# Optimization experiments

Measured on AMD Instinct MI355X. Metric: run time of the kernel, lower is better.

Reference implementation:

```python
import jax, jax.numpy as jnp
import numpy as np
from jax.scipy.special import logsumexp

EPS = 0.05        # entropic regularization (blur^p)
N_ITERS = 20      # Sinkhorn iterations
N, M, D = 8192, 8192, 64


def setup_inputs() -> dict:
    key = jax.random.key(0)
    k1, k2, k3, k4 = jax.random.split(key, 4)
    return {
        "a": jax.random.uniform(k1, (N,), dtype=jnp.float32),
        "x": jax.random.normal(k2, (N, D), dtype=jnp.float32),
        "b": jax.random.uniform(k3, (M,), dtype=jnp.float32),
        "y": jax.random.normal(k4, (M, D), dtype=jnp.float32),
    }


def reference(a, x, b, y):
    eps = EPS
    # _normalize_weights: probability simplex
    a = a / jnp.sum(a)
    b = b / jnp.sum(b)
    loga = jnp.log(a)
    logb = jnp.log(b)
    # squared-Euclidean cost C_ij = ||x_i - y_j||^2, built via one GEMM (online kernel's math)
    x2 = jnp.sum(x * x, axis=1)            # [N]
    y2 = jnp.sum(y * y, axis=1)            # [M]
    C = x2[:, None] + y2[None, :] - 2.0 * (x @ y.T)   # [N, M]

    # log-domain Sinkhorn: f_i = -eps * LSE_j( log b_j + (g_j - C_ij)/eps )
    def softmin_rows(g_, C_, logw):   # reduce over columns j -> [N]
        return -eps * logsumexp(logw[None, :] + (g_[None, :] - C_) / eps, axis=1)

    def softmin_cols(f_, C_, logw):   # reduce over rows i -> [M]
        return -eps * logsumexp(logw[:, None] + (f_[:, None] - C_) / eps, axis=0)

    def body(i, fg):
        f_, g_ = fg
        f_ = softmin_rows(g_, C, logb)
        g_ = softmin_cols(f_, C, loga)
        return (f_, g_)

    f0 = jnp.zeros_like(a)
    g0 = jnp.zeros_like(b)
    f, g = jax.lax.fori_loop(0, N_ITERS, body, (f0, g0))

    # GeomLoss-style: one final symmetric update from detached potentials (Danskin)
    f_d = jax.lax.stop_gradient(f)
    g_d = jax.lax.stop_gradient(g)
    f_fin = softmin_rows(g_d, C, logb)
    g_fin = softmin_cols(f_d, C, loga)
    # OT_eps(a, b) = <a, f> + <b, g>
    return jnp.sum(a * f_fin) + jnp.sum(b * g_fin)
```

## Files before the change

kernel.cpp:

```cpp
#include <hip/hip_runtime.h>
#include <hip/hip_bf16.h>

#define EPS       0.05f
#define N_ITERS   20
#define NR        8192
#define DIM       64
#define LOG2E     1.4426950408889634f
#define LN2       0.6931471805599453f
#define S2        (2.0f * LOG2E / EPS)
#define EPSLN2    (EPS * LN2)
#define NEGINF    (-1e30f)
#define NSPLIT    16

typedef __attribute__((ext_vector_type(8))) short short8;
typedef __attribute__((ext_vector_type(4))) float float4v;

#define GLD_LDS16(src, dst)                                              \
    __builtin_amdgcn_global_load_lds(                                    \
        (const __attribute__((address_space(1))) void*)(src),            \
        (__attribute__((address_space(3))) void*)(dst), 16, 0, 0)

__device__ __forceinline__ float wave_reduce_sum(float v) {
    #pragma unroll
    for (int m = 1; m < 64; m <<= 1) v += __shfl_xor(v, m, 64);
    return v;
}

__device__ __forceinline__ float merge16_l(const float2* __restrict__ P, int i) {
    float2 p[NSPLIT];
    float M = NEGINF;
    #pragma unroll
    for (int k = 0; k < NSPLIT; k++) {
        p[k] = P[k * NR + i];
        M = fmaxf(M, p[k].x);
    }
    float S = 0.f;
    #pragma unroll
    for (int k = 0; k < NSPLIT; k++)
        S += p[k].y * __builtin_amdgcn_exp2f(p[k].x - M);
    return M + __builtin_amdgcn_logf(S);
}

__global__ void sums_kernel(const float* __restrict__ a, const float* __restrict__ b,
                            float* __restrict__ sums) {
    __shared__ float red[32];
    int tid = threadIdx.x;
    float pa = 0.f, pb = 0.f;
    for (int i = tid; i < NR; i += blockDim.x) { pa += a[i]; pb += b[i]; }
    pa = wave_reduce_sum(pa);
    pb = wave_reduce_sum(pb);
    int wid = tid >> 6, ln = tid & 63;
    if (ln == 0) { red[wid] = pa; red[wid + 16] = pb; }
    __syncthreads();
    if (tid == 0) {
        float sa = 0.f, sb = 0.f;
        int nw = blockDim.x >> 6;
        for (int w = 0; w < nw; w++) { sa += red[w]; sb += red[w + 16]; }
        sums[0] = logf(sa); sums[1] = logf(sb); sums[2] = sa; sums[3] = sb;
    }
}

__global__ void prep_kernel(const float* __restrict__ x, const float* __restrict__ y,
                            const float* __restrict__ a, const float* __restrict__ b,
                            const float* __restrict__ sums,
                            short8* __restrict__ xs, short8* __restrict__ ys,
                            float* __restrict__ x2, float* __restrict__ y2,
                            float* __restrict__ la2, float* __restrict__ lb2,
                            float2* __restrict__ Pb) {
    int gid = blockIdx.x * 256 + threadIdx.x;
    bool isx = gid < NR * 8;
    int cid = isx ? gid : gid - NR * 8;
    int row = cid >> 3;
    int c   = cid & 7;
    const float4* src = (const float4*)(isx ? x : y);
    float4 v0 = src[row * 16 + c * 2];
    float4 v1 = src[row * 16 + c * 2 + 1];

    short8 st;
    st[0] = __bfloat16_as_short(__float2bfloat16(v0.x));
    st[1] = __bfloat16_as_short(__float2bfloat16(v0.y));
    st[2] = __bfloat16_as_short(__float2bfloat16(v0.z));
    st[3] = __bfloat16_as_short(__float2bfloat16(v0.w));
    st[4] = __bfloat16_as_short(__float2bfloat16(v1.x));
    st[5] = __bfloat16_as_short(__float2bfloat16(v1.y));
    st[6] = __bfloat16_as_short(__float2bfloat16(v1.z));
    st[7] = __bfloat16_as_short(__float2bfloat16(v1.w));

    int T = row >> 4, ln = row & 15, f = c >> 2, q = c & 3;
    (isx ? xs : ys)[T * 128 + f * 64 + q * 16 + ln] = st;

    float sq = v0.x*v0.x + v0.y*v0.y + v0.z*v0.z + v0.w*v0.w
             + v1.x*v1.x + v1.y*v1.y + v1.z*v1.z + v1.w*v1.w;
    #pragma unroll
    for (int m = 1; m < 8; m <<= 1) sq += __shfl_xor(sq, m, 64);

    if (c == 0) {
        if (isx) {
            x2[row] = sq;
            la2[row] = (logf(a[row]) - sums[0]) * LOG2E;
        } else {
            y2[row] = sq;
            lb2[row] = (logf(b[row]) - sums[1]) * LOG2E;
            Pb[row] = make_float2(sq * (LOG2E / EPS), 1.0f);
            #pragma unroll
            for (int k = 1; k < NSPLIT; k++)
                Pb[k * NR + row] = make_float2(NEGINF, 0.0f);
        }
    }
}

#define LSE4(acc, c4, mm, ss)                                            \
    {                                                                    \
        float z0 = fmaf(S2, (acc)[0], (c4).x);                           \
        float z1 = fmaf(S2, (acc)[1], (c4).y);                           \
        float z2 = fmaf(S2, (acc)[2], (c4).z);                           \
        float z3 = fmaf(S2, (acc)[3], (c4).w);                           \
        float zm = fmaxf(fmaxf(z0, z1), fmaxf(z2, z3));                  \
        float mn = fmaxf((mm), zm);                                      \
        float e  = __builtin_amdgcn_exp2f((mm) - mn);                    \
        float p  = (__builtin_amdgcn_exp2f(z0 - mn)                      \
                  + __builtin_amdgcn_exp2f(z1 - mn))                     \
                 + (__builtin_amdgcn_exp2f(z2 - mn)                      \
                  + __builtin_amdgcn_exp2f(z3 - mn));                    \
        (ss) = fmaf((ss), e, p);                                         \
        (mm) = mn;                                                       \
    }

__global__ __launch_bounds__(1024, 4) void pass_kernel(
        const short8* __restrict__ matXs,
        const short8* __restrict__ matYs,
        const float2* __restrict__ Pin,
        const float* __restrict__ lw2col,
        float2* __restrict__ Pout) {
    __shared__ __attribute__((aligned(16))) char xlds[65536];
    __shared__ __attribute__((aligned(16))) char ybuf[2][16384];
    __shared__ __attribute__((aligned(16))) float cbl[512];
    __shared__ float2 comb[512][5];

    const int tid = threadIdx.x;
    const int bi  = blockIdx.x;
    const int q   = bi & 15;
    const int rg  = bi >> 4;
    const int rb  = rg * 512;
    const int cb0 = q * 512;

    const int w    = tid >> 6;
    const int lane = tid & 63;
    const int quad = lane >> 4;
    const int ln   = lane & 15;
    const int cst  = w & 3;
    const int rq   = w >> 2;

    const char* xsrc = (const char*)matXs + (size_t)rb * 128;
    #pragma unroll
    for (int r = 0; r < 4; r++)
        GLD_LDS16(xsrc + r * 16384 + tid * 16, &xlds[r * 16384 + w * 1024]);
    const char* ysrc = (const char*)matYs + (size_t)cb0 * 128;
    GLD_LDS16(ysrc + 0 * 16384 + tid * 16, &ybuf[0][w * 1024]);
    GLD_LDS16(ysrc + 1 * 16384 + tid * 16, &ybuf[1][w * 1024]);
    __builtin_amdgcn_sched_barrier(0);

    if (tid < 512) {
        int j = cb0 + tid;
        cbl[tid] = lw2col[j] - merge16_l(Pin, j);
    }
    __builtin_amdgcn_sched_barrier(0);
    __builtin_amdgcn_s_waitcnt(0x0071);
    __builtin_amdgcn_s_barrier();
    __builtin_amdgcn_sched_barrier(0);

    short8 xf0[8], xf1[8];
    {
        const char* xw = &xlds[(rq * 8) * 2048];
        #pragma unroll
        for (int t = 0; t < 8; t++) {
            xf0[t] = *(const short8*)(xw + t * 2048 + lane * 16);
            xf1[t] = *(const short8*)(xw + t * 2048 + 1024 + lane * 16);
        }
    }

    float lm[8], ls[8];
    #pragma unroll
    for (int t = 0; t < 8; t++) { lm[t] = NEGINF; ls[t] = 0.f; }

    #pragma unroll
    for (int c = 0; c < 4; c++) {
        const char* base = &ybuf[c & 1][0];
        #pragma unroll
        for (int uu = 0; uu < 2; uu++) {
            const int u = cst * 2 + uu;
            short8 ya0 = *(const short8*)(base + u * 2048 + lane * 16);
            short8 ya1 = *(const short8*)(base + u * 2048 + 1024 + lane * 16);
            float4 c4  = *(const float4*)(cbl + (c * 8 + u) * 16 + quad * 4);

            #pragma unroll
            for (int tt = 0; tt < 8; tt++) {
                float4v acc = {0.f, 0.f, 0.f, 0.f};
                acc = __builtin_amdgcn_mfma_f32_16x16x32_bf16(ya0, xf0[tt], acc, 0, 0, 0);
                acc = __builtin_amdgcn_mfma_f32_16x16x32_bf16(ya1, xf1[tt], acc, 0, 0, 0);
                LSE4(acc, c4, lm[tt], ls[tt]);
            }
        }
        if (c < 3) {
            __builtin_amdgcn_sched_barrier(0);
            __builtin_amdgcn_s_barrier();
            __builtin_amdgcn_sched_barrier(0);
            if (c < 2)
                GLD_LDS16(ysrc + (c + 2) * 16384 + tid * 16, &ybuf[c & 1][w * 1024]);
            __builtin_amdgcn_sched_barrier(0);
            if (c < 2) __builtin_amdgcn_s_waitcnt(0x0071);
            else       __builtin_amdgcn_s_waitcnt(0x0070);
            __builtin_amdgcn_s_barrier();
            __builtin_amdgcn_sched_barrier(0);
        }
    }

    #pragma unroll
    for (int mask = 16; mask < 64; mask <<= 1) {
        #pragma unroll
        for (int t = 0; t < 8; t++) {
            float mo = __shfl_xor(lm[t], mask, 64);
            float so = __shfl_xor(ls[t], mask, 64);
            float M  = fmaxf(lm[t], mo);
            ls[t] = ls[t] * __builtin_amdgcn_exp2f(lm[t] - M)
                  + so    * __builtin_amdgcn_exp2f(mo    - M);
            lm[t] = M;
        }
    }

    __syncthreads();
    if (lane < 16) {
        #pragma unroll
        for (int t = 0; t < 8; t++)
            comb[rq * 128 + t * 16 + ln][cst] = make_float2(lm[t], ls[t]);
    }
    __syncthreads();

    if (tid < 512) {
        float2 cc0 = comb[tid][0];
        float M = cc0.x, S = cc0.y;
        #pragma unroll
        for (int cc = 1; cc < 4; cc++) {
            float2 p = comb[tid][cc];
            float Mn = fmaxf(M, p.x);
            S = S * __builtin_amdgcn_exp2f(M - Mn)
              + p.y * __builtin_amdgcn_exp2f(p.x - Mn);
            M = Mn;
        }
        Pout[q * NR + rb + tid] = make_float2(M, S);
    }
}

__global__ void reduce1_kernel(const float* __restrict__ a, const float* __restrict__ b,
                               const float* __restrict__ x2, const float* __restrict__ y2,
                               const float2* __restrict__ Pff, const float2* __restrict__ Pgf,
                               float2* __restrict__ red2) {
    __shared__ float red[4];
    int tid = threadIdx.x;
    int r   = blockIdx.x * 128 + (tid & 127);
    bool gs = tid >= 128;
    float L  = merge16_l(gs ? Pgf : Pff, r);
    float sq = gs ? y2[r] : x2[r];
    float wv = gs ? b[r]  : a[r];
    float v  = wv * (sq - EPSLN2 * L);
    v = wave_reduce_sum(v);
    if ((tid & 63) == 0) red[tid >> 6] = v;
    __syncthreads();
    if (tid == 0) red2[blockIdx.x] = make_float2(red[0] + red[1], red[2] + red[3]);
}

__global__ void reduce2_kernel(const float* __restrict__ sums,
                               const float2* __restrict__ red2,
                               float* __restrict__ out) {
    int tid = threadIdx.x;
    float2 v = red2[tid];
    float da = wave_reduce_sum(v.x);
    float db = wave_reduce_sum(v.y);
    if (tid == 0) out[0] = da / sums[2] + db / sums[3];
}

extern "C" void kernel_launch(void* const* d_in, const int* in_sizes, int n_in,
                              void* d_out, int out_size, void* d_ws, size_t ws_size,
                              hipStream_t stream) {
    const float* a = (const float*)d_in[0];
    const float* x = (const float*)d_in[1];
    const float* b = (const float*)d_in[2];
    const float* y = (const float*)d_in[3];

    char* ws = (char*)d_ws;
    short8* xs = (short8*)ws;
    short8* ys = (short8*)(ws + (1 << 20));
    float* fp  = (float*)(ws + (2 << 20));
    float* x2  = fp;
    float* y2  = fp + NR;
    float* la2 = fp + 2 * NR;
    float* lb2 = fp + 3 * NR;
    float2* P   = (float2*)(fp + 4 * NR);
    float2* Pf  = P;
    float2* Pb  = P + NSPLIT * NR;
    float2* Pff = P + 2 * NSPLIT * NR;
    float2* Pgf = P + 3 * NSPLIT * NR;
    float2* red2 = P + 4 * NSPLIT * NR;
    float* sums  = (float*)(red2 + 64);

    sums_kernel<<<1, 1024, 0, stream>>>(a, b, sums);
    prep_kernel<<<(2 * NR * 8) / 256, 256, 0, stream>>>(x, y, a, b, sums,
                                                        xs, ys,
                                                        x2, y2, la2, lb2, Pb);

    for (int it = 0; it < N_ITERS; it++) {
        pass_kernel<<<256, 1024, 0, stream>>>(xs, ys, Pb, lb2, Pf);
        pass_kernel<<<256, 1024, 0, stream>>>(ys, xs, Pf, la2, Pb);
    }
    pass_kernel<<<256, 1024, 0, stream>>>(xs, ys, Pb, lb2, Pff);
    pass_kernel<<<256, 1024, 0, stream>>>(ys, xs, Pf, la2, Pgf);

    reduce1_kernel<<<64, 256, 0, stream>>>(a, b, x2, y2, Pff, Pgf, red2);
    reduce2_kernel<<<1, 64, 0, stream>>>(sums, red2, (float*)d_out);
}
```

Before: 859.1 us.

## Precompute column bias in separate merge kernel and triple-buffer Y tiles

The per-column merge of the 16 partial log-sum-exp splits moves out of every pass block into a small merge_kernel. It writes a bias vector that pass_kernel then loads as one float per column. The Y staging buffer grows from two to three slots so three tiles are prefetched up front, and the combine scratch now reuses the X LDS region instead of a separate array. This removes the redundant merge work that all 16 row-group blocks were repeating, and shortens the prologue stall. In exchange it adds 40 extra small kernel launches, and the aliasing of comb onto xlds drops a __syncthreads that previously guarded that region.

```diff
diff --git a/kernel.cpp b/kernel.cpp
--- a/kernel.cpp
+++ b/kernel.cpp
@@ -66,7 +66,7 @@
                             short8* __restrict__ xs, short8* __restrict__ ys,
                             float* __restrict__ x2, float* __restrict__ y2,
                             float* __restrict__ la2, float* __restrict__ lb2,
-                            float2* __restrict__ Pb) {
+                            float* __restrict__ bias_g) {
     int gid = blockIdx.x * 256 + threadIdx.x;
     bool isx = gid < NR * 8;
     int cid = isx ? gid : gid - NR * 8;
@@ -100,13 +100,18 @@
             la2[row] = (logf(a[row]) - sums[0]) * LOG2E;
         } else {
             y2[row] = sq;
-            lb2[row] = (logf(b[row]) - sums[1]) * LOG2E;
-            Pb[row] = make_float2(sq * (LOG2E / EPS), 1.0f);
-            #pragma unroll
-            for (int k = 1; k < NSPLIT; k++)
-                Pb[k * NR + row] = make_float2(NEGINF, 0.0f);
-        }
-    }
+            float lw = (logf(b[row]) - sums[1]) * LOG2E;
+            lb2[row] = lw;
+            bias_g[row] = lw - sq * (LOG2E / EPS);
+        }
+    }
+}
+
+__global__ void merge_kernel(const float2* __restrict__ Pin,
+                             const float* __restrict__ lw2,
+                             float* __restrict__ bias2) {
+    int j = blockIdx.x * 512 + threadIdx.x;
+    bias2[j] = lw2[j] - merge16_l(Pin, j);
 }
 
 #define LSE4(acc, c4, mm, ss)                                            \
@@ -129,13 +134,11 @@
 __global__ __launch_bounds__(1024, 4) void pass_kernel(
         const short8* __restrict__ matXs,
         const short8* __restrict__ matYs,
-        const float2* __restrict__ Pin,
-        const float* __restrict__ lw2col,
+        const float* __restrict__ bias2,
         float2* __restrict__ Pout) {
     __shared__ __attribute__((aligned(16))) char xlds[65536];
-    __shared__ __attribute__((aligned(16))) char ybuf[2][16384];
+    __shared__ __attribute__((aligned(16))) char ybuf[3][16384];
     __shared__ __attribute__((aligned(16))) float cbl[512];
-    __shared__ float2 comb[512][5];
 
     const int tid = threadIdx.x;
     const int bi  = blockIdx.x;
@@ -152,20 +155,22 @@
     const int rq   = w >> 2;
 
     const char* xsrc = (const char*)matXs + (size_t)rb * 128;
+    const char* ysrc = (const char*)matYs + (size_t)cb0 * 128;
     #pragma unroll
     for (int r = 0; r < 4; r++)
         GLD_LDS16(xsrc + r * 16384 + tid * 16, &xlds[r * 16384 + w * 1024]);
-    const char* ysrc = (const char*)matYs + (size_t)cb0 * 128;
     GLD_LDS16(ysrc + 0 * 16384 + tid * 16, &ybuf[0][w * 1024]);
+    __builtin_amdgcn_sched_barrier(0);
+    float bv = bias2[cb0 + (tid & 511)];
+    __builtin_amdgcn_sched_barrier(0);
     GLD_LDS16(ysrc + 1 * 16384 + tid * 16, &ybuf[1][w * 1024]);
-    __builtin_amdgcn_sched_barrier(0);
-
-    if (tid < 512) {
-        int j = cb0 + tid;
-        cbl[tid] = lw2col[j] - merge16_l(Pin, j);
-    }
-    __builtin_amdgcn_sched_barrier(0);
-    __builtin_amdgcn_s_waitcnt(0x0071);
+    GLD_LDS16(ysrc + 2 * 16384 + tid * 16, &ybuf[2][w * 1024]);
+    __builtin_amdgcn_sched_barrier(0);
+
+    if (tid < 512) cbl[tid] = bv;
+    __builtin_amdgcn_sched_barrier(0);
+
+    __builtin_amdgcn_s_waitcnt(0x0072);
     __builtin_amdgcn_s_barrier();
     __builtin_amdgcn_sched_barrier(0);
 
@@ -185,7 +190,7 @@
 
     #pragma unroll
     for (int c = 0; c < 4; c++) {
-        const char* base = &ybuf[c & 1][0];
+        const char* base = &ybuf[c % 3][0];
         #pragma unroll
         for (int uu = 0; uu < 2; uu++) {
             const int u = cst * 2 + uu;
@@ -205,11 +210,12 @@
             __builtin_amdgcn_sched_barrier(0);
             __builtin_amdgcn_s_barrier();
             __builtin_amdgcn_sched_barrier(0);
-            if (c < 2)
-                GLD_LDS16(ysrc + (c + 2) * 16384 + tid * 16, &ybuf[c & 1][w * 1024]);
+            if (c == 0)
+                GLD_LDS16(ysrc + 3 * 16384 + tid * 16, &ybuf[0][w * 1024]);
             __builtin_amdgcn_sched_barrier(0);
-            if (c < 2) __builtin_amdgcn_s_waitcnt(0x0071);
-            else       __builtin_amdgcn_s_waitcnt(0x0070);
+            if (c == 0)      __builtin_amdgcn_s_waitcnt(0x0072);
+            else if (c == 1) __builtin_amdgcn_s_waitcnt(0x0071);
+            else             __builtin_amdgcn_s_waitcnt(0x0070);
             __builtin_amdgcn_s_barrier();
             __builtin_amdgcn_sched_barrier(0);
         }
@@ -228,7 +234,7 @@
         }
     }
 
-    __syncthreads();
+    float2 (*comb)[5] = (float2(*)[5])xlds;
     if (lane < 16) {
         #pragma unroll
         for (int t = 0; t < 8; t++)
@@ -295,7 +301,9 @@
     float* y2  = fp + NR;
     float* la2 = fp + 2 * NR;
     float* lb2 = fp + 3 * NR;
-    float2* P   = (float2*)(fp + 4 * NR);
+    float* bias_f = fp + 4 * NR;
+    float* bias_g = fp + 5 * NR;
+    float2* P   = (float2*)(fp + 6 * NR);
     float2* Pf  = P;
     float2* Pb  = P + NSPLIT * NR;
     float2* Pff = P + 2 * NSPLIT * NR;
@@ -306,14 +314,16 @@
     sums_kernel<<<1, 1024, 0, stream>>>(a, b, sums);
     prep_kernel<<<(2 * NR * 8) / 256, 256, 0, stream>>>(x, y, a, b, sums,
                                                         xs, ys,
-                                                        x2, y2, la2, lb2, Pb);
+                                                        x2, y2, la2, lb2, bias_g);
 
     for (int it = 0; it < N_ITERS; it++) {
-        pass_kernel<<<256, 1024, 0, stream>>>(xs, ys, Pb, lb2, Pf);
-        pass_kernel<<<256, 1024, 0, stream>>>(ys, xs, Pf, la2, Pb);
-    }
-    pass_kernel<<<256, 1024, 0, stream>>>(xs, ys, Pb, lb2, Pff);
-    pass_kernel<<<256, 1024, 0, stream>>>(ys, xs, Pf, la2, Pgf);
+        pass_kernel<<<256, 1024, 0, stream>>>(xs, ys, bias_g, Pf);
+        merge_kernel<<<16, 512, 0, stream>>>(Pf, la2, bias_f);
+        pass_kernel<<<256, 1024, 0, stream>>>(ys, xs, bias_f, Pb);
+        merge_kernel<<<16, 512, 0, stream>>>(Pb, lb2, bias_g);
+    }
+    pass_kernel<<<256, 1024, 0, stream>>>(xs, ys, bias_g, Pff);
+    pass_kernel<<<256, 1024, 0, stream>>>(ys, xs, bias_f, Pgf);
 
     reduce1_kernel<<<64, 256, 0, stream>>>(a, b, x2, y2, Pff, Pgf, red2);
     reduce2_kernel<<<1, 64, 0, stream>>>(sums, red2, (float*)d_out);
```

After: 927.3 us. 1.08x slower.

## Triple-buffer Y tiles and parallelize prologue partial-LSE merge across all threads

Applied to the files above, without the earlier changes.

Adds a third Y LDS buffer so three column chunks are prefetched up front, with fewer mid-loop barriers waiting on loads. The prologue merge of the 16 partial (max,sum) pairs now uses all 1024 threads: each half merges 8 partials in registers, and the two halves are combined through LDS. Those Pin loads are issued before the async LDS copies so their latency overlaps. The final combine scratch reuses the X LDS region to stay within the shared-memory budget. The risk is in the hand-tuned waitcnt values, which must match the new order of memory operations.

```diff
diff --git a/kernel.cpp b/kernel.cpp
--- a/kernel.cpp
+++ b/kernel.cpp
@@ -133,9 +133,9 @@
         const float* __restrict__ lw2col,
         float2* __restrict__ Pout) {
     __shared__ __attribute__((aligned(16))) char xlds[65536];
-    __shared__ __attribute__((aligned(16))) char ybuf[2][16384];
+    __shared__ __attribute__((aligned(16))) char ybuf[3][16384];
     __shared__ __attribute__((aligned(16))) float cbl[512];
-    __shared__ float2 comb[512][5];
+    __shared__ __attribute__((aligned(16))) float2 pm[1024];
 
     const int tid = threadIdx.x;
     const int bi  = blockIdx.x;
@@ -151,21 +151,53 @@
     const int cst  = w & 3;
     const int rq   = w >> 2;
 
+    const int jcol = cb0 + (tid & 511);
+    const int hh   = tid >> 9;
+    float2 pp[8];
+    #pragma unroll
+    for (int k = 0; k < 8; k++)
+        pp[k] = Pin[(hh * 8 + k) * NR + jcol];
+    float lwv = lw2col[jcol];
+    __builtin_amdgcn_sched_barrier(0);
+
     const char* xsrc = (const char*)matXs + (size_t)rb * 128;
+    const char* ysrc = (const char*)matYs + (size_t)cb0 * 128;
     #pragma unroll
     for (int r = 0; r < 4; r++)
         GLD_LDS16(xsrc + r * 16384 + tid * 16, &xlds[r * 16384 + w * 1024]);
-    const char* ysrc = (const char*)matYs + (size_t)cb0 * 128;
     GLD_LDS16(ysrc + 0 * 16384 + tid * 16, &ybuf[0][w * 1024]);
     GLD_LDS16(ysrc + 1 * 16384 + tid * 16, &ybuf[1][w * 1024]);
+    GLD_LDS16(ysrc + 2 * 16384 + tid * 16, &ybuf[2][w * 1024]);
+    __builtin_amdgcn_sched_barrier(0);
+
+    __builtin_amdgcn_s_waitcnt(0x0077);
+    __builtin_amdgcn_sched_barrier(0);
+
+    {
+        float M = pp[0].x;
+        #pragma unroll
+        for (int k = 1; k < 8; k++) M = fmaxf(M, pp[k].x);
+        float S = 0.f;
+        #pragma unroll
+        for (int k = 0; k < 8; k++)
+            S += pp[k].y * __builtin_amdgcn_exp2f(pp[k].x - M);
+        pm[tid] = make_float2(M, S);
+    }
+    __builtin_amdgcn_sched_barrier(0);
+    __builtin_amdgcn_s_waitcnt(0xC07F);
+    __builtin_amdgcn_s_barrier();
     __builtin_amdgcn_sched_barrier(0);
 
     if (tid < 512) {
-        int j = cb0 + tid;
-        cbl[tid] = lw2col[j] - merge16_l(Pin, j);
-    }
-    __builtin_amdgcn_sched_barrier(0);
-    __builtin_amdgcn_s_waitcnt(0x0071);
+        float2 h0 = pm[tid];
+        float2 h1 = pm[tid + 512];
+        float M = fmaxf(h0.x, h1.x);
+        float S = h0.y * __builtin_amdgcn_exp2f(h0.x - M)
+                + h1.y * __builtin_amdgcn_exp2f(h1.x - M);
+        cbl[tid] = lwv - (M + __builtin_amdgcn_logf(S));
+    }
+    __builtin_amdgcn_sched_barrier(0);
+    __builtin_amdgcn_s_waitcnt(0x0072);
     __builtin_amdgcn_s_barrier();
     __builtin_amdgcn_sched_barrier(0);
 
@@ -185,7 +217,7 @@
 
     #pragma unroll
     for (int c = 0; c < 4; c++) {
-        const char* base = &ybuf[c & 1][0];
+        const char* base = &ybuf[c % 3][0];
         #pragma unroll
         for (int uu = 0; uu < 2; uu++) {
             const int u = cst * 2 + uu;
@@ -205,11 +237,12 @@
             __builtin_amdgcn_sched_barrier(0);
             __builtin_amdgcn_s_barrier();
             __builtin_amdgcn_sched_barrier(0);
-            if (c < 2)
-                GLD_LDS16(ysrc + (c + 2) * 16384 + tid * 16, &ybuf[c & 1][w * 1024]);
+            if (c == 0)
+                GLD_LDS16(ysrc + 3 * 16384 + tid * 16, &ybuf[0][w * 1024]);
             __builtin_amdgcn_sched_barrier(0);
-            if (c < 2) __builtin_amdgcn_s_waitcnt(0x0071);
-            else       __builtin_amdgcn_s_waitcnt(0x0070);
+            if (c == 0)      __builtin_amdgcn_s_waitcnt(0x0072);
+            else if (c == 1) __builtin_amdgcn_s_waitcnt(0x0071);
+            else             __builtin_amdgcn_s_waitcnt(0x0070);
             __builtin_amdgcn_s_barrier();
             __builtin_amdgcn_sched_barrier(0);
         }
@@ -228,6 +261,7 @@
         }
     }
 
+    float2 (*comb)[5] = (float2(*)[5])xlds;
     __syncthreads();
     if (lane < 16) {
         #pragma unroll
```

Measured after the change: 875.6 us. About the same (+1.9%).
